# Performance work log

Measured on AMD Instinct MI355X. Metric: run time of the kernel, lower is better.

The kernel has to match this reference:

```python
import jax, jax.numpy as jnp
import numpy as np


def setup_inputs() -> dict:
    key = jax.random.key(0)
    k = jax.random.split(key, 6)
    B = 65536
    return {
        "x": jax.random.normal(k[0], (B, 784), dtype=jnp.float32),
        "conv_w": jax.random.normal(k[1], (3, 3), dtype=jnp.float32),
        "fc1_w": jax.random.normal(k[2], (128, 676), dtype=jnp.float32) * 0.04,
        "fc1_b": jax.random.normal(k[3], (128,), dtype=jnp.float32),
        "fc2_w": jax.random.normal(k[4], (10, 128), dtype=jnp.float32) * 0.09,
        "fc2_b": jax.random.normal(k[5], (10,), dtype=jnp.float32),
    }


def reference(x, conv_w, fc1_w, fc1_b, fc2_w, fc2_b):
    B = x.shape[0]
    img = x.reshape(B, 1, 28, 28)  # NCHW, single channel
    # Valid cross-correlation with a 3x3 kernel (matches the torch sum(region*weight) loop)
    kern = conv_w.reshape(1, 1, 3, 3)  # OIHW
    conv = jax.lax.conv_general_dilated(
        img, kern, window_strides=(1, 1), padding="VALID",
        dimension_numbers=("NCHW", "OIHW", "NCHW"))  # [B,1,26,26]
    h = conv.reshape(B, 26 * 26)
    h = jax.nn.relu(h @ fc1_w.T + fc1_b)  # [B,128]
    logits = h @ fc2_w.T + fc2_b  # [B,10]
    return logits
```

## Files before the change

kernel.cpp:

```cpp
#include <hip/hip_runtime.h>

typedef __bf16 bf16x8 __attribute__((ext_vector_type(8)));
typedef float  f32x4  __attribute__((ext_vector_type(4)));

#define KDIM    784
#define KSTEP   32
#define NSTEPS  25
#define NCOLS   128
#define NT      8
#define WAVES   4
#define ROWS_PER_WAVE 32
#define ROWS_PER_BLOCK (WAVES * ROWS_PER_WAVE)
#define STAGE_BYTES 16384
#define HSH_PAD 132
#define HCHUNK  16

__global__ __launch_bounds__(64) void prep_weff(
    const float* __restrict__ conv_w,
    const float* __restrict__ fc1_w,
    __bf16* __restrict__ wfrag)
{
  int idx = blockIdx.x * 64 + threadIdx.x;
  if (idx >= NSTEPS * NT * 64) return;
  int lane = idx & 63;
  int n    = (idx >> 6) & (NT - 1);
  int s    = idx >> 9;
  int col  = n * 16 + (lane & 15);
  int kb   = s * KSTEP + (lane >> 4) * 8;
  bf16x8 o;
#pragma unroll
  for (int j = 0; j < 8; ++j) {
    int k = kb + j;
    float v = 0.f;
    if (k < KDIM) {
      int r = k / 28, c = k % 28;
#pragma unroll
      for (int u = 0; u < 3; ++u)
#pragma unroll
        for (int w = 0; w < 3; ++w) {
          int p = r - u, q = c - w;
          if (p >= 0 && p < 26 && q >= 0 && q < 26)
            v = fmaf(conv_w[u * 3 + w], fc1_w[col * 676 + p * 26 + q], v);
        }
    }
    o[j] = (__bf16)v;
  }
  reinterpret_cast<bf16x8*>(wfrag)[idx] = o;
}

__device__ __forceinline__ bf16x8 pack8(f32x4 lo, f32x4 hi) {
  bf16x8 r;
  r[0] = (__bf16)lo[0]; r[1] = (__bf16)lo[1];
  r[2] = (__bf16)lo[2]; r[3] = (__bf16)lo[3];
  r[4] = (__bf16)hi[0]; r[5] = (__bf16)hi[1];
  r[6] = (__bf16)hi[2]; r[7] = (__bf16)hi[3];
  return r;
}

__device__ __forceinline__ void split8(f32x4 a, f32x4 b, bf16x8& hi, bf16x8& lo) {
#pragma unroll
  for (int j = 0; j < 4; ++j) {
    __bf16 h = (__bf16)a[j]; hi[j] = h; lo[j] = (__bf16)(a[j] - (float)h);
  }
#pragma unroll
  for (int j = 0; j < 4; ++j) {
    __bf16 h = (__bf16)b[j]; hi[4 + j] = h; lo[4 + j] = (__bf16)(b[j] - (float)h);
  }
}

__device__ __forceinline__ void stage_issue(
    const __bf16* __restrict__ wfrag, unsigned char* dstbuf,
    int stage, int wave, int lane, int nchunks)
{
#pragma unroll
  for (int c = 0; c < 4; ++c) {
    int cw = wave * 4 + c;
    if (cw < nchunks) {
      const unsigned char* src =
          (const unsigned char*)wfrag + (size_t)stage * STAGE_BYTES + cw * 1024 + lane * 16;
      unsigned char* dst = dstbuf + cw * 1024 + lane * 16;
      __builtin_amdgcn_global_load_lds(
          (const __attribute__((address_space(1))) unsigned int*)src,
          (__attribute__((address_space(3))) unsigned int*)dst,
          16, 0, 0);
    }
  }
}

__global__ __launch_bounds__(256, 3) void fused_mlp(
    const float*  __restrict__ x,
    const __bf16* __restrict__ wfrag,
    const float*  __restrict__ fc1_b,
    const float*  __restrict__ fc2_w,
    const float*  __restrict__ fc2_b,
    float*        __restrict__ out)
{
  __shared__ __align__(16) unsigned char smem[WAVES * HCHUNK * HSH_PAD * 4];
  float (*hsh)[HCHUNK][HSH_PAD] =
      reinterpret_cast<float (*)[HCHUNK][HSH_PAD]>(smem);

  int tid  = threadIdx.x;
  int wave = tid >> 6, lane = tid & 63;
  int lrow = lane & 15;
  int lgrp = lane >> 4;
  long wrow0 = (long)blockIdx.x * ROWS_PER_BLOCK + wave * ROWS_PER_WAVE;

  const float* xr0 = x + (wrow0 + lrow) * KDIM;
  const float* xr1 = xr0 + 16 * KDIM;

  f32x4 acc[2][NT];
#pragma unroll
  for (int m = 0; m < 2; ++m)
#pragma unroll
    for (int n = 0; n < NT; ++n) acc[m][n] = (f32x4){0.f, 0.f, 0.f, 0.f};

  f32x4 xv[8];
#define LOAD_STAGE(T)                                          \
  {                                                            \
    int k0 = (2 * (T)) * KSTEP + lgrp * 8;                     \
    xv[0] = *(const f32x4*)(xr0 + k0);                         \
    xv[1] = *(const f32x4*)(xr0 + k0 + 4);                     \
    xv[2] = *(const f32x4*)(xr1 + k0);                         \
    xv[3] = *(const f32x4*)(xr1 + k0 + 4);                     \
    xv[4] = *(const f32x4*)(xr0 + k0 + KSTEP);                 \
    xv[5] = *(const f32x4*)(xr0 + k0 + KSTEP + 4);             \
    xv[6] = *(const f32x4*)(xr1 + k0 + KSTEP);                 \
    xv[7] = *(const f32x4*)(xr1 + k0 + KSTEP + 4);             \
  }

  stage_issue(wfrag, smem, 0, wave, lane, 16);
  LOAD_STAGE(0);
  int cur = 0;

  for (int t = 0; t < 12; ++t) {
    __syncthreads();
    stage_issue(wfrag, smem + (cur ^ 1) * STAGE_BYTES, t + 1, wave, lane,
                (t < 11) ? 16 : 8);

    bf16x8 a00 = pack8(xv[0], xv[1]), a01 = pack8(xv[2], xv[3]);
    bf16x8 a10 = pack8(xv[4], xv[5]), a11 = pack8(xv[6], xv[7]);

    if (t < 11) {
      LOAD_STAGE(t + 1);
    } else {
      if (lgrp < 2) {
        int k = (NSTEPS - 1) * KSTEP + lgrp * 8;
        xv[0] = *(const f32x4*)(xr0 + k);
        xv[1] = *(const f32x4*)(xr0 + k + 4);
        xv[2] = *(const f32x4*)(xr1 + k);
        xv[3] = *(const f32x4*)(xr1 + k + 4);
      } else {
        xv[0] = (f32x4){0.f,0.f,0.f,0.f}; xv[1] = (f32x4){0.f,0.f,0.f,0.f};
        xv[2] = (f32x4){0.f,0.f,0.f,0.f}; xv[3] = (f32x4){0.f,0.f,0.f,0.f};
      }
    }

    const bf16x8* bp = (const bf16x8*)(smem + cur * STAGE_BYTES) + lane;
    {
      bf16x8 bf[NT];
#pragma unroll
      for (int n = 0; n < NT; ++n) bf[n] = bp[n * 64];
#pragma unroll
      for (int n = 0; n < NT; ++n) {
        acc[0][n] = __builtin_amdgcn_mfma_f32_16x16x32_bf16(a00, bf[n], acc[0][n], 0, 0, 0);
        acc[1][n] = __builtin_amdgcn_mfma_f32_16x16x32_bf16(a01, bf[n], acc[1][n], 0, 0, 0);
      }
    }
    {
      bf16x8 bf[NT];
#pragma unroll
      for (int n = 0; n < NT; ++n) bf[n] = bp[512 + n * 64];
#pragma unroll
      for (int n = 0; n < NT; ++n) {
        acc[0][n] = __builtin_amdgcn_mfma_f32_16x16x32_bf16(a10, bf[n], acc[0][n], 0, 0, 0);
        acc[1][n] = __builtin_amdgcn_mfma_f32_16x16x32_bf16(a11, bf[n], acc[1][n], 0, 0, 0);
      }
    }
    cur ^= 1;
  }

  __syncthreads();
  {
    bf16x8 a0 = pack8(xv[0], xv[1]);
    bf16x8 a1 = pack8(xv[2], xv[3]);
    const bf16x8* bp = (const bf16x8*)(smem + cur * STAGE_BYTES) + lane;
#pragma unroll
    for (int n = 0; n < NT; ++n) {
      bf16x8 b = bp[n * 64];
      acc[0][n] = __builtin_amdgcn_mfma_f32_16x16x32_bf16(a0, b, acc[0][n], 0, 0, 0);
      acc[1][n] = __builtin_amdgcn_mfma_f32_16x16x32_bf16(a1, b, acc[1][n], 0, 0, 0);
    }
  }
  __syncthreads();

  int osafe = (lrow < 10) ? lrow : 9;
  bf16x8 whi[4], wlo[4];
#pragma unroll
  for (int s2 = 0; s2 < 4; ++s2) {
    f32x4 w0 = *(const f32x4*)(fc2_w + osafe * NCOLS + s2 * 32 + lgrp * 8);
    f32x4 w1 = *(const f32x4*)(fc2_w + osafe * NCOLS + s2 * 32 + lgrp * 8 + 4);
    if (lrow >= 10) { w0 = (f32x4){0.f,0.f,0.f,0.f}; w1 = (f32x4){0.f,0.f,0.f,0.f}; }
    split8(w0, w1, whi[s2], wlo[s2]);
  }
  float b2 = (lrow < 10) ? fc2_b[lrow] : 0.f;
  float bcol[NT];
#pragma unroll
  for (int n = 0; n < NT; ++n) bcol[n] = fc1_b[n * 16 + lrow];

#pragma unroll
  for (int m2 = 0; m2 < 2; ++m2) {
#pragma unroll
    for (int n = 0; n < NT; ++n) {
      int col = n * 16 + lrow;
#pragma unroll
      for (int ri = 0; ri < 4; ++ri) {
        int rl = lgrp * 4 + ri;
        hsh[wave][rl][col] = fmaxf(acc[m2][n][ri] + bcol[n], 0.f);
      }
    }
    f32x4 acc2 = (f32x4){0.f, 0.f, 0.f, 0.f};
    const float* hr = &hsh[wave][lrow][0];
#pragma unroll
    for (int s2 = 0; s2 < 4; ++s2) {
      f32x4 h0 = *(const f32x4*)(hr + s2 * 32 + lgrp * 8);
      f32x4 h1 = *(const f32x4*)(hr + s2 * 32 + lgrp * 8 + 4);
      bf16x8 ahi, alo; split8(h0, h1, ahi, alo);
      acc2 = __builtin_amdgcn_mfma_f32_16x16x32_bf16(ahi, whi[s2], acc2, 0, 0, 0);
      acc2 = __builtin_amdgcn_mfma_f32_16x16x32_bf16(ahi, wlo[s2], acc2, 0, 0, 0);
      acc2 = __builtin_amdgcn_mfma_f32_16x16x32_bf16(alo, whi[s2], acc2, 0, 0, 0);
    }
    if (lrow < 10) {
#pragma unroll
      for (int ri = 0; ri < 4; ++ri)
        out[(wrow0 + m2 * 16 + lgrp * 4 + ri) * 10 + lrow] = acc2[ri] + b2;
    }
  }
}

extern "C" void kernel_launch(void* const* d_in, const int* in_sizes, int n_in,
                              void* d_out, int out_size, void* d_ws, size_t ws_size,
                              hipStream_t stream) {
  const float* x      = (const float*)d_in[0];
  const float* conv_w = (const float*)d_in[1];
  const float* fc1_w  = (const float*)d_in[2];
  const float* fc1_b  = (const float*)d_in[3];
  const float* fc2_w  = (const float*)d_in[4];
  const float* fc2_b  = (const float*)d_in[5];
  float* outp = (float*)d_out;
  __bf16* wfrag = (__bf16*)d_ws;

  int Btotal = in_sizes[0] / KDIM;
  int prep_threads = NSTEPS * NT * 64;

  hipLaunchKernelGGL(prep_weff, dim3(prep_threads / 64), dim3(64), 0, stream,
                     conv_w, fc1_w, wfrag);
  hipLaunchKernelGGL(fused_mlp, dim3(Btotal / ROWS_PER_BLOCK), dim3(256), 0, stream,
                     x, wfrag, fc1_b, fc2_w, fc2_b, outp);
}
```

Measured before the change: 49.21 us.

## Stage activation tiles through swizzled LDS with async global-to-LDS copies

Activations are no longer loaded from global memory into registers. Each step now copies a 128-row by 32-column tile of x into a double-buffered, XOR-swizzled LDS region using global_load_lds, alongside the weight fragments. The k-step shrinks to one 32-wide MFMA step per iteration. The goal is to move the large activation stream onto asynchronous DMA-style copies and free registers. In exchange, LDS use grows to 48KB per block, occupancy drops to two blocks per CU, and there are twice as many barriers.

```diff
diff --git a/kernel.cpp b/kernel.cpp
--- a/kernel.cpp
+++ b/kernel.cpp
@@ -11,7 +11,8 @@
 #define WAVES   4
 #define ROWS_PER_WAVE 32
 #define ROWS_PER_BLOCK (WAVES * ROWS_PER_WAVE)
-#define STAGE_BYTES 16384
+#define XSTEP_BYTES 16384
+#define WSTEP_BYTES 8192
 #define HSH_PAD 132
 #define HCHUNK  16
 
@@ -68,26 +69,38 @@
   }
 }
 
-__device__ __forceinline__ void stage_issue(
-    const __bf16* __restrict__ wfrag, unsigned char* dstbuf,
-    int stage, int wave, int lane, int nchunks)
+__device__ __forceinline__ void stage_copy(
+    const float* __restrict__ xrowbase, const __bf16* __restrict__ wfrag,
+    unsigned char* smem, int buf, int t, int wave, int lane)
 {
-#pragma unroll
-  for (int c = 0; c < 4; ++c) {
-    int cw = wave * 4 + c;
-    if (cw < nchunks) {
-      const unsigned char* src =
-          (const unsigned char*)wfrag + (size_t)stage * STAGE_BYTES + cw * 1024 + lane * 16;
-      unsigned char* dst = dstbuf + cw * 1024 + lane * 16;
-      __builtin_amdgcn_global_load_lds(
-          (const __attribute__((address_space(1))) unsigned int*)src,
-          (__attribute__((address_space(3))) unsigned int*)dst,
-          16, 0, 0);
-    }
-  }
-}
-
-__global__ __launch_bounds__(256, 3) void fused_mlp(
+  unsigned char* xdst = smem + buf * XSTEP_BYTES;
+  int sb = ((lane & 7) * 16) ^ (((lane >> 3) & 7) << 4);
+  int row_off = t * 128 + sb;
+  if (row_off + 16 > KDIM * 4) row_off = 0;
+#pragma unroll
+  for (int i = 0; i < 4; ++i) {
+    int c = wave * 4 + i;
+    const unsigned char* src =
+        (const unsigned char*)(xrowbase + (size_t)(c * 8 + (lane >> 3)) * KDIM) + row_off;
+    unsigned char* dst = xdst + c * 1024 + lane * 16;
+    __builtin_amdgcn_global_load_lds(
+        (const __attribute__((address_space(1))) unsigned int*)src,
+        (__attribute__((address_space(3))) unsigned int*)dst, 16, 0, 0);
+  }
+  unsigned char* wdst = smem + 2 * XSTEP_BYTES + buf * WSTEP_BYTES;
+  const unsigned char* wsrc = (const unsigned char*)wfrag + (size_t)t * WSTEP_BYTES;
+#pragma unroll
+  for (int i = 0; i < 2; ++i) {
+    int c = wave * 2 + i;
+    const unsigned char* src = wsrc + c * 1024 + lane * 16;
+    unsigned char* dst = wdst + c * 1024 + lane * 16;
+    __builtin_amdgcn_global_load_lds(
+        (const __attribute__((address_space(1))) unsigned int*)src,
+        (__attribute__((address_space(3))) unsigned int*)dst, 16, 0, 0);
+  }
+}
+
+__global__ __launch_bounds__(256, 2) void fused_mlp(
     const float*  __restrict__ x,
     const __bf16* __restrict__ wfrag,
     const float*  __restrict__ fc1_b,
@@ -95,7 +108,7 @@
     const float*  __restrict__ fc2_b,
     float*        __restrict__ out)
 {
-  __shared__ __align__(16) unsigned char smem[WAVES * HCHUNK * HSH_PAD * 4];
+  __shared__ __align__(16) unsigned char smem[2 * XSTEP_BYTES + 2 * WSTEP_BYTES];
   float (*hsh)[HCHUNK][HSH_PAD] =
       reinterpret_cast<float (*)[HCHUNK][HSH_PAD]>(smem);
 
@@ -104,9 +117,7 @@
   int lrow = lane & 15;
   int lgrp = lane >> 4;
   long wrow0 = (long)blockIdx.x * ROWS_PER_BLOCK + wave * ROWS_PER_WAVE;
-
-  const float* xr0 = x + (wrow0 + lrow) * KDIM;
-  const float* xr1 = xr0 + 16 * KDIM;
+  const float* xrowbase = x + (long)blockIdx.x * ROWS_PER_BLOCK * KDIM;
 
   f32x4 acc[2][NT];
 #pragma unroll
@@ -114,81 +125,38 @@
 #pragma unroll
     for (int n = 0; n < NT; ++n) acc[m][n] = (f32x4){0.f, 0.f, 0.f, 0.f};
 
-  f32x4 xv[8];
-#define LOAD_STAGE(T)                                          \
-  {                                                            \
-    int k0 = (2 * (T)) * KSTEP + lgrp * 8;                     \
-    xv[0] = *(const f32x4*)(xr0 + k0);                         \
-    xv[1] = *(const f32x4*)(xr0 + k0 + 4);                     \
-    xv[2] = *(const f32x4*)(xr1 + k0);                         \
-    xv[3] = *(const f32x4*)(xr1 + k0 + 4);                     \
-    xv[4] = *(const f32x4*)(xr0 + k0 + KSTEP);                 \
-    xv[5] = *(const f32x4*)(xr0 + k0 + KSTEP + 4);             \
-    xv[6] = *(const f32x4*)(xr1 + k0 + KSTEP);                 \
-    xv[7] = *(const f32x4*)(xr1 + k0 + KSTEP + 4);             \
-  }
-
-  stage_issue(wfrag, smem, 0, wave, lane, 16);
-  LOAD_STAGE(0);
-  int cur = 0;
-
-  for (int t = 0; t < 12; ++t) {
+  int base0 = (wave * 32 + lrow) * 128;
+  int base1 = base0 + 16 * 128;
+  int swz   = (lrow & 7) << 4;
+  int sb0   = (lgrp * 32) ^ swz;
+  int sb1   = (lgrp * 32 + 16) ^ swz;
+
+  stage_copy(xrowbase, wfrag, smem, 0, 0, wave, lane);
+
+  for (int t = 0; t < NSTEPS; ++t) {
     __syncthreads();
-    stage_issue(wfrag, smem + (cur ^ 1) * STAGE_BYTES, t + 1, wave, lane,
-                (t < 11) ? 16 : 8);
-
-    bf16x8 a00 = pack8(xv[0], xv[1]), a01 = pack8(xv[2], xv[3]);
-    bf16x8 a10 = pack8(xv[4], xv[5]), a11 = pack8(xv[6], xv[7]);
-
-    if (t < 11) {
-      LOAD_STAGE(t + 1);
-    } else {
-      if (lgrp < 2) {
-        int k = (NSTEPS - 1) * KSTEP + lgrp * 8;
-        xv[0] = *(const f32x4*)(xr0 + k);
-        xv[1] = *(const f32x4*)(xr0 + k + 4);
-        xv[2] = *(const f32x4*)(xr1 + k);
-        xv[3] = *(const f32x4*)(xr1 + k + 4);
-      } else {
-        xv[0] = (f32x4){0.f,0.f,0.f,0.f}; xv[1] = (f32x4){0.f,0.f,0.f,0.f};
-        xv[2] = (f32x4){0.f,0.f,0.f,0.f}; xv[3] = (f32x4){0.f,0.f,0.f,0.f};
-      }
-    }
-
-    const bf16x8* bp = (const bf16x8*)(smem + cur * STAGE_BYTES) + lane;
-    {
-      bf16x8 bf[NT];
-#pragma unroll
-      for (int n = 0; n < NT; ++n) bf[n] = bp[n * 64];
-#pragma unroll
-      for (int n = 0; n < NT; ++n) {
-        acc[0][n] = __builtin_amdgcn_mfma_f32_16x16x32_bf16(a00, bf[n], acc[0][n], 0, 0, 0);
-        acc[1][n] = __builtin_amdgcn_mfma_f32_16x16x32_bf16(a01, bf[n], acc[1][n], 0, 0, 0);
-      }
-    }
-    {
-      bf16x8 bf[NT];
-#pragma unroll
-      for (int n = 0; n < NT; ++n) bf[n] = bp[512 + n * 64];
-#pragma unroll
-      for (int n = 0; n < NT; ++n) {
-        acc[0][n] = __builtin_amdgcn_mfma_f32_16x16x32_bf16(a10, bf[n], acc[0][n], 0, 0, 0);
-        acc[1][n] = __builtin_amdgcn_mfma_f32_16x16x32_bf16(a11, bf[n], acc[1][n], 0, 0, 0);
-      }
-    }
-    cur ^= 1;
-  }
-
-  __syncthreads();
-  {
-    bf16x8 a0 = pack8(xv[0], xv[1]);
-    bf16x8 a1 = pack8(xv[2], xv[3]);
-    const bf16x8* bp = (const bf16x8*)(smem + cur * STAGE_BYTES) + lane;
+    if (t < NSTEPS - 1)
+      stage_copy(xrowbase, wfrag, smem, (t + 1) & 1, t + 1, wave, lane);
+
+    int buf = t & 1;
+    const unsigned char* xb = smem + buf * XSTEP_BYTES;
+    const bf16x8* bp =
+        (const bf16x8*)(smem + 2 * XSTEP_BYTES + buf * WSTEP_BYTES) + lane;
+
+    f32x4 x00 = *(const f32x4*)(xb + base0 + sb0);
+    f32x4 x01 = *(const f32x4*)(xb + base0 + sb1);
+    f32x4 x10 = *(const f32x4*)(xb + base1 + sb0);
+    f32x4 x11 = *(const f32x4*)(xb + base1 + sb1);
+    bf16x8 a0 = pack8(x00, x01);
+    bf16x8 a1 = pack8(x10, x11);
+
+    bf16x8 bf[NT];
+#pragma unroll
+    for (int n = 0; n < NT; ++n) bf[n] = bp[n * 64];
 #pragma unroll
     for (int n = 0; n < NT; ++n) {
-      bf16x8 b = bp[n * 64];
-      acc[0][n] = __builtin_amdgcn_mfma_f32_16x16x32_bf16(a0, b, acc[0][n], 0, 0, 0);
-      acc[1][n] = __builtin_amdgcn_mfma_f32_16x16x32_bf16(a1, b, acc[1][n], 0, 0, 0);
+      acc[0][n] = __builtin_amdgcn_mfma_f32_16x16x32_bf16(a0, bf[n], acc[0][n], 0, 0, 0);
+      acc[1][n] = __builtin_amdgcn_mfma_f32_16x16x32_bf16(a1, bf[n], acc[1][n], 0, 0, 0);
     }
   }
   __syncthreads();
```

Result: faster. 46.99 us, median of 2 (-4.5%).
